# Performance work log

Measured on AMD Instinct MI355X. Metric: run time of the kernel, lower is better.

The kernel has to match this reference:

```python
import jax, jax.numpy as jnp
import numpy as np

H = 8      # n_heads
DK = 64    # d_k per head
EPS = 1e-5       # InstanceNorm1d eps
SLOPE = 0.01     # LeakyReLU negative slope


def setup_inputs() -> dict:
    key = jax.random.key(0)
    ks = jax.random.split(key, 6)
    B, C, L = 16, 256, 1024
    HD = H * DK  # 512
    return {
        "x": jax.random.normal(ks[0], (B, C, L), dtype=jnp.float32),
        "Wq": jax.random.normal(ks[1], (HD, C), dtype=jnp.float32) * 0.02,
        "Wk": jax.random.normal(ks[2], (HD, C), dtype=jnp.float32) * 0.02,
        "Wv": jax.random.normal(ks[3], (HD, C), dtype=jnp.float32) * 0.02,
        "Wo": jax.random.normal(ks[4], (C, HD), dtype=jnp.float32) * 0.02,
        "gamma": jax.random.normal(ks[5], (1,), dtype=jnp.float32),
    }


def reference(x, Wq, Wk, Wv, Wo, gamma):
    B, C, L = x.shape
    # conv1x1 projections (bias=False) == channel matmuls -> [B, H*DK, L]
    # then reshape/permute into heads: [B, H, L, DK]
    def proj(W):
        y = jnp.einsum('oc,bcl->bol', W, x)          # [B, H*DK, L]
        return y.reshape(B, H, DK, L).transpose(0, 1, 3, 2)  # [B, H, L, DK]

    q, k, v = proj(Wq), proj(Wk), proj(Wv)
    # softmax-free linear attention: (Q K^T / d_k) V
    logits = jnp.einsum('bhld,bhmd->bhlm', q, k) / DK  # [B, H, L, L]
    out = jnp.einsum('bhlm,bhmd->bhld', logits, v)     # [B, H, L, DK]
    # merge heads back to channel-first [B, H*DK, L]
    merged = out.transpose(0, 1, 3, 2).reshape(B, H * DK, L)
    # output conv1x1 -> [B, C, L]
    o = jnp.einsum('oc,bcl->bol', Wo, merged)
    # InstanceNorm1d (affine=False): normalize over L per (b, c)
    mu = jnp.mean(o, axis=-1, keepdims=True)
    var = jnp.var(o, axis=-1, keepdims=True)
    o = (o - mu) * jax.lax.rsqrt(var + EPS)
    # gamma-scaled residual + LeakyReLU
    y = o * gamma + x
    return jnp.where(y >= 0, y, SLOPE * y)
```

## Files before the change

kernel.cpp:

```cpp
#include <hip/hip_runtime.h>

typedef __bf16 bf16;
typedef bf16 bf16x8 __attribute__((ext_vector_type(8)));
typedef bf16 bf16x4 __attribute__((ext_vector_type(4)));
typedef float f32x4 __attribute__((ext_vector_type(4)));

#define EPS 1e-5f
#define SLOPE 0.01f

__device__ __forceinline__ void gld_lds16(const bf16* g, bf16* l) {
    __builtin_amdgcn_global_load_lds(
        (const __attribute__((address_space(1))) unsigned int*)g,
        (__attribute__((address_space(3))) unsigned int*)l, 16, 0, 0);
}

__global__ __launch_bounds__(256) void prep_kernel(
    const float* __restrict__ x,
    const float* __restrict__ Wq, const float* __restrict__ Wk,
    const float* __restrict__ Wv, const float* __restrict__ Wo,
    bf16* __restrict__ xT, bf16* __restrict__ xB,
    bf16* __restrict__ WkB, bf16* __restrict__ WvB,
    bf16* __restrict__ WoB, bf16* __restrict__ WqT)
{
    __shared__ float tile[64][65];
    const int id = blockIdx.x;
    const int t = threadIdx.x;
    if (id < 1024) {
        const int lt = id & 15, ct = (id >> 4) & 3, b = id >> 6;
        {
            const int cl = t >> 2;
            const int l4 = (t & 3) << 4;
            const float* src = x + (size_t)(b * 256 + ct * 64 + cl) * 1024 + lt * 64 + l4;
            float4 v0 = ((const float4*)src)[0];
            float4 v1 = ((const float4*)src)[1];
            float4 v2 = ((const float4*)src)[2];
            float4 v3 = ((const float4*)src)[3];
            bf16x8 r0, r1;
            r0[0]=(bf16)v0.x; r0[1]=(bf16)v0.y; r0[2]=(bf16)v0.z; r0[3]=(bf16)v0.w;
            r0[4]=(bf16)v1.x; r0[5]=(bf16)v1.y; r0[6]=(bf16)v1.z; r0[7]=(bf16)v1.w;
            r1[0]=(bf16)v2.x; r1[1]=(bf16)v2.y; r1[2]=(bf16)v2.z; r1[3]=(bf16)v2.w;
            r1[4]=(bf16)v3.x; r1[5]=(bf16)v3.y; r1[6]=(bf16)v3.z; r1[7]=(bf16)v3.w;
            bf16* xbd = xB + (size_t)(b * 256 + ct * 64 + cl) * 1024 + lt * 64 + l4;
            *(bf16x8*)xbd = r0;
            *(bf16x8*)(xbd + 8) = r1;
            float* tr = &tile[cl][l4];
            tr[0]=v0.x; tr[1]=v0.y; tr[2]=v0.z; tr[3]=v0.w;
            tr[4]=v1.x; tr[5]=v1.y; tr[6]=v1.z; tr[7]=v1.w;
            tr[8]=v2.x; tr[9]=v2.y; tr[10]=v2.z; tr[11]=v2.w;
            tr[12]=v3.x; tr[13]=v3.y; tr[14]=v3.z; tr[15]=v3.w;
        }
        __syncthreads();
        {
            const int lw = t >> 2;
            const int ec = (t & 3) << 4;
            bf16x8 o0, o1;
            #pragma unroll
            for (int ii = 0; ii < 8; ++ii) {
                o0[ii] = (bf16)tile[ec + ii][lw];
                o1[ii] = (bf16)tile[ec + 8 + ii][lw];
            }
            bf16* dst = xT + (size_t)(b * 1024 + lt * 64 + lw) * 256 + ct * 64 + ec;
            *(bf16x8*)dst = o0;
            *(bf16x8*)(dst + 8) = o1;
        }
    } else if (id < 1408) {
        const int i = (id - 1024) * 1024 + t * 4;
        const float* src; bf16* dst;
        if (i < 131072)      { src = Wk + i;            dst = WkB + i; }
        else if (i < 262144) { src = Wv + (i - 131072); dst = WvB + (i - 131072); }
        else                 { src = Wo + (i - 262144); dst = WoB + (i - 262144); }
        float4 v = *(const float4*)src;
        bf16x4 o;
        o[0]=(bf16)v.x; o[1]=(bf16)v.y; o[2]=(bf16)v.z; o[3]=(bf16)v.w;
        *(bf16x4*)dst = o;
    } else {
        const int id2 = id - 1408;
        const int h = id2 >> 2, ct = id2 & 3;
        {
            const int e  = t >> 2;
            const int c4 = (t & 3) << 4;
            const float* src = Wq + (size_t)(h * 64 + e) * 256 + ct * 64 + c4;
            float4 v0 = ((const float4*)src)[0];
            float4 v1 = ((const float4*)src)[1];
            float4 v2 = ((const float4*)src)[2];
            float4 v3 = ((const float4*)src)[3];
            float* tr = &tile[e][c4];
            tr[0]=v0.x; tr[1]=v0.y; tr[2]=v0.z; tr[3]=v0.w;
            tr[4]=v1.x; tr[5]=v1.y; tr[6]=v1.z; tr[7]=v1.w;
            tr[8]=v2.x; tr[9]=v2.y; tr[10]=v2.z; tr[11]=v2.w;
            tr[12]=v3.x; tr[13]=v3.y; tr[14]=v3.z; tr[15]=v3.w;
        }
        __syncthreads();
        {
            const int c  = t >> 2;
            const int e4 = (t & 3) << 4;
            bf16x8 o0, o1;
            #pragma unroll
            for (int ii = 0; ii < 8; ++ii) {
                o0[ii] = (bf16)tile[e4 + ii][c];
                o1[ii] = (bf16)tile[e4 + 8 + ii][c];
            }
            bf16* dst = WqT + (size_t)h * 16384 + (size_t)(ct * 64 + c) * 64 + e4;
            *(bf16x8*)dst = o0;
            *(bf16x8*)(dst + 8) = o1;
        }
    }
}

template<int KDIM, typename OutT>
__global__ __launch_bounds__(256) void gemm128_bt(
    const bf16* __restrict__ A, const bf16* __restrict__ Bt, OutT* __restrict__ C,
    long long sA, long long sBt, long long sC, int ldC)
{
    constexpr int NT = KDIM / 32;
    constexpr int NB = 5;
    __shared__ bf16 As[NB][128 * 32];
    __shared__ bf16 Bs[NB][128 * 32];
    const int z = blockIdx.z;
    A  += (size_t)z * sA;
    Bt += (size_t)z * sBt;
    C  += (size_t)z * sC;
    const int m0 = blockIdx.x * 128;
    const int n0 = blockIdx.y * 128;
    const int t = threadIdx.x, w = t >> 6, l = t & 63;
    const int srow = w * 16 + (l >> 2);
    const int ske  = (l & 3) * 8;
    const bf16* ga = A  + (size_t)(m0 + srow) * KDIM + ske;
    const bf16* gb = Bt + (size_t)(n0 + srow) * KDIM + ske;
    const int loff = srow * 32 + ske;
    const int lm = l & 15, lq = l >> 4;
    const int wm = (w & 1) * 64, wn = (w >> 1) * 64;

    #pragma unroll
    for (int i = 0; i < NB - 1; ++i) {
        const int k0 = i * 32;
        gld_lds16(ga + k0, &As[i][0] + loff);
        gld_lds16(ga + k0 + (size_t)64 * KDIM, &As[i][0] + 64 * 32 + loff);
        gld_lds16(gb + k0, &Bs[i][0] + loff);
        gld_lds16(gb + k0 + (size_t)64 * KDIM, &Bs[i][0] + 64 * 32 + loff);
    }

    f32x4 acc[4][4] = {};
    #pragma unroll
    for (int kt = 0; kt < NT; ++kt) {
        const int cur = kt % NB;
        const int stg = (kt + NB - 1) % NB;
        const int remain = NT - 1 - kt;
        if (remain >= 3)      asm volatile("s_waitcnt vmcnt(12)" ::: "memory");
        else if (remain == 2) asm volatile("s_waitcnt vmcnt(8)"  ::: "memory");
        else if (remain == 1) asm volatile("s_waitcnt vmcnt(4)"  ::: "memory");
        else                  asm volatile("s_waitcnt vmcnt(0)"  ::: "memory");
        __builtin_amdgcn_s_barrier();
        __builtin_amdgcn_sched_barrier(0);
        if (kt + NB - 1 < NT) {
            const int k0 = (kt + NB - 1) * 32;
            gld_lds16(ga + k0, &As[stg][0] + loff);
            gld_lds16(ga + k0 + (size_t)64 * KDIM, &As[stg][0] + 64 * 32 + loff);
            gld_lds16(gb + k0, &Bs[stg][0] + loff);
            gld_lds16(gb + k0 + (size_t)64 * KDIM, &Bs[stg][0] + 64 * 32 + loff);
        }
        bf16x8 af[4], bfr[4];
        #pragma unroll
        for (int i = 0; i < 4; ++i)
            af[i] = *(const bf16x8*)(&As[cur][0] + (wm + i * 16 + lm) * 32 + lq * 8);
        #pragma unroll
        for (int j = 0; j < 4; ++j)
            bfr[j] = *(const bf16x8*)(&Bs[cur][0] + (wn + j * 16 + lm) * 32 + lq * 8);
        #pragma unroll
        for (int i = 0; i < 4; ++i)
            #pragma unroll
            for (int j = 0; j < 4; ++j)
                acc[i][j] = __builtin_amdgcn_mfma_f32_16x16x32_bf16(af[i], bfr[j], acc[i][j], 0, 0, 0);
    }
    #pragma unroll
    for (int i = 0; i < 4; ++i)
        #pragma unroll
        for (int j = 0; j < 4; ++j) {
            const int row = m0 + wm + i * 16 + lq * 4;
            const int col = n0 + wn + j * 16 + lm;
            OutT* cp = C + (size_t)row * ldC + col;
            #pragma unroll
            for (int r = 0; r < 4; ++r)
                cp[(size_t)r * ldC] = (OutT)acc[i][j][r];
        }
}

template<int KDIM, typename OutT>
__global__ __launch_bounds__(256) void gemm64_bt(
    const bf16* __restrict__ A, const bf16* __restrict__ Bt, OutT* __restrict__ C,
    long long sA, long long sBt, long long sC, int ldC)
{
    constexpr int NT = KDIM / 32;
    constexpr int NB = 5;
    __shared__ bf16 As[NB][64 * 32];
    __shared__ bf16 Bs[NB][64 * 32];
    const int z = blockIdx.z;
    A  += (size_t)z * sA;
    Bt += (size_t)z * sBt;
    C  += (size_t)z * sC;
    const int m0 = blockIdx.x * 64;
    const int n0 = blockIdx.y * 64;
    const int t = threadIdx.x, w = t >> 6, l = t & 63;
    const int srow = t >> 2;
    const int ske  = (t & 3) * 8;
    const bf16* ga = A  + (size_t)(m0 + srow) * KDIM + ske;
    const bf16* gb = Bt + (size_t)(n0 + srow) * KDIM + ske;
    const int loff = srow * 32 + ske;
    const int lm = l & 15, lq = l >> 4;

    #pragma unroll
    for (int i = 0; i < NB - 1; ++i) {
        const int k0 = i * 32;
        gld_lds16(ga + k0, &As[i][0] + loff);
        gld_lds16(gb + k0, &Bs[i][0] + loff);
    }

    f32x4 acc[4] = {};
    #pragma unroll
    for (int kt = 0; kt < NT; ++kt) {
        const int cur = kt % NB;
        const int stg = (kt + NB - 1) % NB;
        const int remain = NT - 1 - kt;
        if (remain >= 3)      asm volatile("s_waitcnt vmcnt(6)" ::: "memory");
        else if (remain == 2) asm volatile("s_waitcnt vmcnt(4)" ::: "memory");
        else if (remain == 1) asm volatile("s_waitcnt vmcnt(2)" ::: "memory");
        else                  asm volatile("s_waitcnt vmcnt(0)" ::: "memory");
        __builtin_amdgcn_s_barrier();
        __builtin_amdgcn_sched_barrier(0);
        if (kt + NB - 1 < NT) {
            const int k0 = (kt + NB - 1) * 32;
            gld_lds16(ga + k0, &As[stg][0] + loff);
            gld_lds16(gb + k0, &Bs[stg][0] + loff);
        }
        bf16x8 af = *(const bf16x8*)(&As[cur][0] + (w * 16 + lm) * 32 + lq * 8);
        bf16x8 bfr[4];
        #pragma unroll
        for (int j = 0; j < 4; ++j)
            bfr[j] = *(const bf16x8*)(&Bs[cur][0] + (j * 16 + lm) * 32 + lq * 8);
        #pragma unroll
        for (int j = 0; j < 4; ++j)
            acc[j] = __builtin_amdgcn_mfma_f32_16x16x32_bf16(af, bfr[j], acc[j], 0, 0, 0);
    }
    #pragma unroll
    for (int j = 0; j < 4; ++j) {
        const int row = m0 + w * 16 + lq * 4;
        const int col = n0 + j * 16 + lm;
        OutT* cp = C + (size_t)row * ldC + col;
        #pragma unroll
        for (int r = 0; r < 4; ++r)
            cp[(size_t)r * ldC] = (OutT)acc[j][r];
    }
}

struct __align__(16) Tm2Ph1 { bf16 P[16384]; bf16 Va[16384]; bf16 Gr[4][8192]; };
struct __align__(16) Tm2Ph2 { bf16 P[16384]; bf16 Kc[16384]; bf16 Qb[16384]; bf16 Tb[4096]; };
union  __align__(16) Tm2Sm  { Tm2Ph1 p1; Tm2Ph2 p2; };

__global__ __launch_bounds__(256) void tm2_kernel(
    const bf16* __restrict__ G, const bf16* __restrict__ WvB,
    const bf16* __restrict__ WkB, const bf16* __restrict__ WqT,
    bf16* __restrict__ WmT)
{
    __shared__ Tm2Sm sm;
    const int bh = blockIdx.x;
    const int b = bh >> 3, h = bh & 7;
    const bf16* Gg = G   + (size_t)b * 65536;
    const bf16* Vg = WvB + (size_t)h * 16384;
    const bf16* Kg = WkB + (size_t)h * 16384;
    const bf16* Qg = WqT + (size_t)h * 16384;
    const int t = threadIdx.x, w = t >> 6, l = t & 63;
    const int lm = l & 15, lq = l >> 4;

    {
        const int rb = t >> 2 << 2;
    }
    #pragma unroll
    for (int it = 0; it < 4; ++it) {
        const int idx = it * 256 + t;
        const int r = idx >> 2, s2 = idx & 3;
        gld_lds16(Gg + (size_t)r * 256 + 0 * 32 + (s2 ^ (r & 3)) * 8,
                  &sm.p1.Gr[0][0] + r * 32 + s2 * 8);
    }
    #pragma unroll
    for (int it = 0; it < 8; ++it) {
        const int idx = it * 256 + t;
        const int r = idx >> 5, s = idx & 31;
        gld_lds16(Vg + (size_t)r * 256 + (s ^ (r & 7)) * 8,
                  sm.p1.Va + r * 256 + s * 8);
    }
    #pragma unroll
    for (int tb = 1; tb < 3; ++tb) {
        #pragma unroll
        for (int it = 0; it < 4; ++it) {
            const int idx = it * 256 + t;
            const int r = idx >> 2, s2 = idx & 3;
            gld_lds16(Gg + (size_t)r * 256 + tb * 32 + (s2 ^ (r & 3)) * 8,
                      &sm.p1.Gr[tb][0] + r * 32 + s2 * 8);
        }
    }

    f32x4 accP[4][4] = {};
    #pragma unroll
    for (int kt = 0; kt < 8; ++kt) {
        if (kt <= 5)      asm volatile("s_waitcnt vmcnt(8)" ::: "memory");
        else if (kt == 6) asm volatile("s_waitcnt vmcnt(4)" ::: "memory");
        else              asm volatile("s_waitcnt vmcnt(0)" ::: "memory");
        __builtin_amdgcn_s_barrier();
        __builtin_amdgcn_sched_barrier(0);
        if (kt < 5) {
            const int tb = kt + 3;
            #pragma unroll
            for (int it = 0; it < 4; ++it) {
                const int idx = it * 256 + t;
                const int r = idx >> 2, s2 = idx & 3;
                gld_lds16(Gg + (size_t)r * 256 + tb * 32 + (s2 ^ (r & 3)) * 8,
                          &sm.p1.Gr[tb & 3][0] + r * 32 + s2 * 8);
            }
        }
        bf16x8 af[4], bfr[4];
        #pragma unroll
        for (int mf = 0; mf < 4; ++mf) {
            const int ra = mf * 16 + lm;
            af[mf] = *(const bf16x8*)(sm.p1.Va + ra * 256 + ((kt * 4 + lq) ^ (ra & 7)) * 8);
        }
        #pragma unroll
        for (int nf = 0; nf < 4; ++nf) {
            const int rb = w * 64 + nf * 16 + lm;
            bfr[nf] = *(const bf16x8*)(&sm.p1.Gr[kt & 3][0] + rb * 32 + (lq ^ (rb & 3)) * 8);
        }
        #pragma unroll
        for (int mf = 0; mf < 4; ++mf)
            #pragma unroll
            for (int nf = 0; nf < 4; ++nf)
                accP[mf][nf] = __builtin_amdgcn_mfma_f32_16x16x32_bf16(af[mf], bfr[nf], accP[mf][nf], 0, 0, 0);
    }
    #pragma unroll
    for (int mf = 0; mf < 4; ++mf)
        #pragma unroll
        for (int nf = 0; nf < 4; ++nf)
            #pragma unroll
            for (int ri = 0; ri < 4; ++ri) {
                const int d = mf * 16 + lq * 4 + ri;
                const int c = w * 64 + nf * 16 + lm;
                sm.p1.P[d * 256 + (((c >> 3) ^ (d & 7)) << 3) + (c & 7)] =
                    (bf16)accP[mf][nf][ri];
            }
    __syncthreads();

    #pragma unroll
    for (int it = 0; it < 8; ++it) {
        const int idx = it * 256 + t;
        const int r = idx >> 5, s = idx & 31;
        gld_lds16(Kg + (size_t)r * 256 + (s ^ (r & 7)) * 8,
                  sm.p2.Kc + r * 256 + s * 8);
    }
    #pragma unroll
    for (int it = 0; it < 8; ++it) {
        const int idx = it * 256 + t;
        const int r = idx >> 3, s2 = idx & 7;
        gld_lds16(Qg + (size_t)r * 64 + (s2 ^ (r & 7)) * 8,
                  sm.p2.Qb + r * 64 + s2 * 8);
    }

    asm volatile("s_waitcnt vmcnt(8)" ::: "memory");
    __builtin_amdgcn_s_barrier();
    __builtin_amdgcn_sched_barrier(0);
    f32x4 accT[4] = {};
    #pragma unroll
    for (int kk = 0; kk < 8; ++kk) {
        const int ra = w * 16 + lm;
        bf16x8 a = *(const bf16x8*)(sm.p2.P + ra * 256 + ((kk * 4 + lq) ^ (ra & 7)) * 8);
        #pragma unroll
        for (int nf = 0; nf < 4; ++nf) {
            const int rb = nf * 16 + lm;
            bf16x8 bb = *(const bf16x8*)(sm.p2.Kc + rb * 256 + ((kk * 4 + lq) ^ (rb & 7)) * 8);
            accT[nf] = __builtin_amdgcn_mfma_f32_16x16x32_bf16(a, bb, accT[nf], 0, 0, 0);
        }
    }
    #pragma unroll
    for (int nf = 0; nf < 4; ++nf)
        #pragma unroll
        for (int ri = 0; ri < 4; ++ri) {
            const int row = w * 16 + lq * 4 + ri;
            const int col = nf * 16 + lm;
            sm.p2.Tb[row * 64 + (((col >> 3) ^ (row & 7)) << 3) + (col & 7)] =
                (bf16)(accT[nf][ri] * 0.015625f);
        }
    asm volatile("s_waitcnt vmcnt(0)" ::: "memory");
    __syncthreads();

    f32x4 accM[4][4] = {};
    #pragma unroll
    for (int ks = 0; ks < 2; ++ks) {
        const int q = ks * 4 + lq;
        bf16x8 bfrag[4];
        #pragma unroll
        for (int nf = 0; nf < 4; ++nf) {
            const int rb = nf * 16 + lm;
            bfrag[nf] = *(const bf16x8*)(sm.p2.Tb + rb * 64 + (q ^ (rb & 7)) * 8);
        }
        #pragma unroll
        for (int mf = 0; mf < 4; ++mf) {
            const int ra = w * 64 + mf * 16 + lm;
            bf16x8 a = *(const bf16x8*)(sm.p2.Qb + ra * 64 + (q ^ (ra & 7)) * 8);
            #pragma unroll
            for (int nf = 0; nf < 4; ++nf)
                accM[mf][nf] = __builtin_amdgcn_mfma_f32_16x16x32_bf16(a, bfrag[nf], accM[mf][nf], 0, 0, 0);
        }
    }
    bf16* Wg = WmT + (size_t)b * 131072 + h * 64;
    #pragma unroll
    for (int mf = 0; mf < 4; ++mf)
        #pragma unroll
        for (int nf = 0; nf < 4; ++nf)
            #pragma unroll
            for (int ri = 0; ri < 4; ++ri) {
                const int c = w * 64 + mf * 16 + lq * 4 + ri;
                const int d = nf * 16 + lm;
                Wg[(size_t)c * 512 + d] = (bf16)accM[mf][nf][ri];
            }
}

__global__ __launch_bounds__(256) void norm_kernel(
    const bf16* __restrict__ o, const bf16* __restrict__ xB,
    const float* __restrict__ gamma, float* __restrict__ y)
{
    const size_t row = blockIdx.x;
    const bf16* orow = o + row * 1024;
    const bf16* xrow = xB + row * 1024;
    float* yrow = y + row * 1024;
    const int tid = threadIdx.x;

    bf16x4 ov = *(const bf16x4*)(orow + tid * 4);
    float4 v = {(float)ov[0], (float)ov[1], (float)ov[2], (float)ov[3]};
    float s  = v.x + v.y + v.z + v.w;
    float ss = v.x * v.x + v.y * v.y + v.z * v.z + v.w * v.w;
    #pragma unroll
    for (int off = 32; off > 0; off >>= 1) {
        s  += __shfl_down(s, off);
        ss += __shfl_down(ss, off);
    }
    __shared__ float red[10];
    const int wave = tid >> 6, lane = tid & 63;
    if (lane == 0) { red[wave] = s; red[4 + wave] = ss; }
    __syncthreads();
    if (tid == 0) {
        float a  = red[0] + red[1] + red[2] + red[3];
        float b2 = red[4] + red[5] + red[6] + red[7];
        float mu = a * (1.0f / 1024.0f);
        float var = b2 * (1.0f / 1024.0f) - mu * mu;
        red[8] = mu;
        red[9] = rsqrtf(var + EPS);
    }
    __syncthreads();
    const float mu = red[8], inv = red[9], g = gamma[0];
    bf16x4 xv4 = *(const bf16x4*)(xrow + tid * 4);
    float4 r;
    r.x = (v.x - mu) * inv * g + (float)xv4[0];
    r.y = (v.y - mu) * inv * g + (float)xv4[1];
    r.z = (v.z - mu) * inv * g + (float)xv4[2];
    r.w = (v.w - mu) * inv * g + (float)xv4[3];
    r.x = r.x >= 0.f ? r.x : SLOPE * r.x;
    r.y = r.y >= 0.f ? r.y : SLOPE * r.y;
    r.z = r.z >= 0.f ? r.z : SLOPE * r.z;
    r.w = r.w >= 0.f ? r.w : SLOPE * r.w;
    ((float4*)yrow)[tid] = r;
}

extern "C" void kernel_launch(void* const* d_in, const int* in_sizes, int n_in,
                              void* d_out, int out_size, void* d_ws, size_t ws_size,
                              hipStream_t stream) {
    const float* x     = (const float*)d_in[0];
    const float* Wq    = (const float*)d_in[1];
    const float* Wk    = (const float*)d_in[2];
    const float* Wv    = (const float*)d_in[3];
    const float* Wo    = (const float*)d_in[4];
    const float* gamma = (const float*)d_in[5];
    float* y = (float*)d_out;

    char* wsb = (char*)d_ws;
    bf16* xT  = (bf16*)(wsb);
    bf16* xB  = (bf16*)(wsb +  8388608);
    bf16* WkB = (bf16*)(wsb + 16777216);
    bf16* WvB = (bf16*)(wsb + 17039360);
    bf16* WoB = (bf16*)(wsb + 17301504);
    bf16* WqT = (bf16*)(wsb + 17563648);
    bf16* G   = (bf16*)(wsb + 17825792);
    bf16* WmT = (bf16*)(wsb + 24117248);
    bf16* Wt  = (bf16*)(wsb + 28311552);
    bf16* o   = (bf16*)(wsb + 30408704);

    prep_kernel<<<dim3(1440), 256, 0, stream>>>(x, Wq, Wk, Wv, Wo, xT, xB, WkB, WvB, WoB, WqT);

    gemm64_bt<1024, bf16><<<dim3(4, 4, 16), 256, 0, stream>>>(
        xB, xB, G, 262144LL, 262144LL, 65536LL, 256);

    tm2_kernel<<<dim3(128), 256, 0, stream>>>(G, WvB, WkB, WqT, WmT);

    gemm64_bt<512, bf16><<<dim3(4, 4, 16), 256, 0, stream>>>(
        WoB, WmT, Wt, 0LL, 131072LL, 65536LL, 256);

    gemm128_bt<256, bf16><<<dim3(2, 8, 16), 256, 0, stream>>>(
        Wt, xT, o, 65536LL, 262144LL, 262144LL, 1024);

    norm_kernel<<<dim3(4096), 256, 0, stream>>>(o, xB, gamma, y);
}
```

Before: 122.7 us.

## Remap block indices so all tiles of one batch land on the same XCD

Adds an XCD-aware block index decode: blocks are dispatched round-robin across 8 XCDs, so raw id & 7 picks the XCD. The decode assigns all tiles of one batch (or batch-head) to a single XCD. This is applied to the prep, all GEMMs, tm2 and norm kernels, and the 3D grids are flattened to 1D. The goal is better L2 reuse of per-batch operands shared across tiles within an XCD, at the cost of extra index arithmetic and possible load imbalance.

Measured after the change: 120.7 us. Within noise of the previous version (-1.6%).

```diff
diff --git a/kernel.cpp b/kernel.cpp
--- a/kernel.cpp
+++ b/kernel.cpp
@@ -12,6 +12,13 @@
     __builtin_amdgcn_global_load_lds(
         (const __attribute__((address_space(1))) unsigned int*)g,
         (__attribute__((address_space(3))) unsigned int*)l, 16, 0, 0);
+}
+
+template<int LOG2T>
+__device__ __forceinline__ void xcd_decode(int raw, int& b, int& t) {
+    const int p = raw & 7, m = raw >> 3;
+    b = ((m >> LOG2T) << 3) + p;
+    t = m & ((1 << LOG2T) - 1);
 }
 
 __global__ __launch_bounds__(256) void prep_kernel(
@@ -23,7 +30,12 @@
     bf16* __restrict__ WoB, bf16* __restrict__ WqT)
 {
     __shared__ float tile[64][65];
-    const int id = blockIdx.x;
+    const int raw = blockIdx.x;
+    int id;
+    if (raw < 1024) {
+        int b, t64; xcd_decode<6>(raw, b, t64);
+        id = (b << 6) | t64;
+    } else id = raw;
     const int t = threadIdx.x;
     if (id < 1024) {
         const int lt = id & 15, ct = (id >> 4) & 3, b = id >> 6;
@@ -116,12 +128,12 @@
     constexpr int NB = 5;
     __shared__ bf16 As[NB][128 * 32];
     __shared__ bf16 Bs[NB][128 * 32];
-    const int z = blockIdx.z;
+    int z, tt; xcd_decode<4>(blockIdx.x, z, tt);
     A  += (size_t)z * sA;
     Bt += (size_t)z * sBt;
     C  += (size_t)z * sC;
-    const int m0 = blockIdx.x * 128;
-    const int n0 = blockIdx.y * 128;
+    const int m0 = (tt >> 3) * 128;
+    const int n0 = (tt & 7) * 128;
     const int t = threadIdx.x, w = t >> 6, l = t & 63;
     const int srow = w * 16 + (l >> 2);
     const int ske  = (l & 3) * 8;
@@ -194,12 +206,12 @@
     constexpr int NB = 5;
     __shared__ bf16 As[NB][64 * 32];
     __shared__ bf16 Bs[NB][64 * 32];
-    const int z = blockIdx.z;
+    int z, tt; xcd_decode<4>(blockIdx.x, z, tt);
     A  += (size_t)z * sA;
     Bt += (size_t)z * sBt;
     C  += (size_t)z * sC;
-    const int m0 = blockIdx.x * 64;
-    const int n0 = blockIdx.y * 64;
+    const int m0 = (tt & 3) * 64;
+    const int n0 = (tt >> 2) * 64;
     const int t = threadIdx.x, w = t >> 6, l = t & 63;
     const int srow = t >> 2;
     const int ske  = (t & 3) * 8;
@@ -262,8 +274,7 @@
     bf16* __restrict__ WmT)
 {
     __shared__ Tm2Sm sm;
-    const int bh = blockIdx.x;
-    const int b = bh >> 3, h = bh & 7;
+    int b, h; xcd_decode<3>(blockIdx.x, b, h);
     const bf16* Gg = G   + (size_t)b * 65536;
     const bf16* Vg = WvB + (size_t)h * 16384;
     const bf16* Kg = WkB + (size_t)h * 16384;
@@ -271,9 +282,6 @@
     const int t = threadIdx.x, w = t >> 6, l = t & 63;
     const int lm = l & 15, lq = l >> 4;
 
-    {
-        const int rb = t >> 2 << 2;
-    }
     #pragma unroll
     for (int it = 0; it < 4; ++it) {
         const int idx = it * 256 + t;
@@ -425,7 +433,8 @@
     const bf16* __restrict__ o, const bf16* __restrict__ xB,
     const float* __restrict__ gamma, float* __restrict__ y)
 {
-    const size_t row = blockIdx.x;
+    int b, c; xcd_decode<8>(blockIdx.x, b, c);
+    const size_t row = ((size_t)b << 8) | c;
     const bf16* orow = o + row * 1024;
     const bf16* xrow = xB + row * 1024;
     float* yrow = y + row * 1024;
@@ -492,15 +501,15 @@
 
     prep_kernel<<<dim3(1440), 256, 0, stream>>>(x, Wq, Wk, Wv, Wo, xT, xB, WkB, WvB, WoB, WqT);
 
-    gemm64_bt<1024, bf16><<<dim3(4, 4, 16), 256, 0, stream>>>(
+    gemm64_bt<1024, bf16><<<dim3(256), 256, 0, stream>>>(
         xB, xB, G, 262144LL, 262144LL, 65536LL, 256);
 
     tm2_kernel<<<dim3(128), 256, 0, stream>>>(G, WvB, WkB, WqT, WmT);
 
-    gemm64_bt<512, bf16><<<dim3(4, 4, 16), 256, 0, stream>>>(
+    gemm64_bt<512, bf16><<<dim3(256), 256, 0, stream>>>(
         WoB, WmT, Wt, 0LL, 131072LL, 65536LL, 256);
 
-    gemm128_bt<256, bf16><<<dim3(2, 8, 16), 256, 0, stream>>>(
+    gemm128_bt<256, bf16><<<dim3(256), 256, 0, stream>>>(
         Wt, xT, o, 65536LL, 262144LL, 262144LL, 1024);
 
     norm_kernel<<<dim3(4096), 256, 0, stream>>>(o, xB, gamma, y);
```
